# Kernel tuning notes

Hardware: AMD Instinct MI355X
Metric: run time of the kernel (lower is better)

The kernel has to match this reference:

```python
import jax, jax.numpy as jnp
import numpy as np

NB = 5  # number of graph nodes per image
COUNT_THRESH = 10000  # min pixel count for a region to be selected
BOX_DOWNSCALE = 16.0  # backbone stride


def _masks_to_boxes(mask_np, ids):
    # torchvision.ops.masks_to_boxes: (xmin, ymin, xmax, ymax) in pixel coords
    boxes = []
    for oid in ids:
        ys, xs = np.nonzero(mask_np == oid)
        boxes.append([xs.min(), ys.min(), xs.max(), ys.max()])
    return np.asarray(boxes, dtype=np.float32)


def _select_boxes(seg_logits):
    # mask = espnet(x).max(1)[1]; original code only keeps boxes from the LAST
    # batch element (loop variable overwritten each iteration) -- preserved here.
    mask = np.asarray(jnp.argmax(seg_logits, axis=1))[-1]
    ids, counts = np.unique(mask, return_counts=True)
    ids, counts = ids[1:], counts[1:]  # drop background / first label
    boxes = _masks_to_boxes(mask, ids) / BOX_DOWNSCALE  # feature-map coords
    # rr = argsort(argsort(counts, descending)) == rank of each region by size
    rr = np.argsort(np.argsort(-counts))
    sel = []
    for idx in range(len(boxes)):
        for b_idx in range(len(rr)):
            if idx == rr[b_idx] and counts[b_idx] > COUNT_THRESH and len(sel) < NB - 2:
                sel.append(b_idx)
                break
    return boxes.astype(np.int64), sel


def setup_inputs() -> dict:
    key = jax.random.key(0)
    k1, k2, k3 = jax.random.split(key, 3)
    N, K, Hin, Win = 4, 20, 480, 640   # even H/W -> parity padding is a no-op
    C, H, W = 512, Hin // 16, Win // 16  # stride-16 VGG backbone features
    return {
        "seg_logits": jax.random.normal(k1, (N, K, Hin, Win), jnp.float32),
        "feat": jax.random.normal(k2, (N, C, H, W), jnp.float32),
        "pool_x": jax.random.normal(k3, (N, C), jnp.float32),
    }


def reference(seg_logits, feat, pool_x):
    boxes, sel = _select_boxes(seg_logits)
    N, C, H, W = feat.shape
    # Selected-region crops; boxes identical for every batch element (original
    # bug), so each crop+resize is vectorized over the batch dim.
    nodes = []
    for b in sel:
        x0, y0, x1, y1 = [int(v) for v in boxes[b]]
        crop = feat[:, :, y0:y1, x0:x1]
        nodes.append(jax.image.resize(crop, (N, C, H, W), "bilinear"))
    # Fixed fallback boxes (center, left/top/right/bottom strips)
    bb = [[W // 4, H // 4, 3 * W // 4, 3 * H // 4],
          [0, 0, W // 3, H],
          [0, 0, W, H // 3],
          [2 * W // 3, 0, W, H],
          [0, 2 * H // 3, W, H]]
    if len(nodes) < NB:
        for i in range(len(bb) - len(nodes)):  # range evaluated once, as in original
            x0, y0, x1, y1 = bb[i]
            crop = feat[:, :, y0:y1, x0:x1]
            nodes.append(jax.image.resize(crop, (N, C, H, W), "bilinear"))
    graph_nodes = jnp.stack(nodes, axis=1)  # [N, NB, C, H, W]
    # Original: graph_nodes.view(NB, N, ...) is a raw reshape, then cat with feat
    x_cropped = jnp.concatenate(
        [graph_nodes.reshape(NB, N, C, H, W), feat[None]], axis=0)  # [NB+1,N,C,H,W]
    return pool_x, NB, N, x_cropped
```

## Files before the change

kernel.cpp:

```cpp
#include <hip/hip_runtime.h>
#include <hip/hip_bf16.h>

#define K_CLS 20
#define HIN 480
#define WIN 640
#define NPIX (HIN * WIN)
#define C_ 512
#define H_ 30
#define W_ 40
#define NB_ 5
#define CNT_THRESH 10000
#define XCROP_ELEMS (6 * 4 * C_ * H_ * W_)
#define OUT_TOTAL (2050 + XCROP_ELEMS)
#define NPAIR (OUT_TOTAL / 2)

#define NBLK_STATS 300
#define NODE_OFF (NBLK_STATS * 100)


__global__ void stats_k(const float* __restrict__ seg, int* __restrict__ ws) {
    __shared__ int s_cnt[K_CLS], s_mnx[K_CLS], s_mny[K_CLS], s_mxx[K_CLS], s_mxy[K_CLS];
    int t = threadIdx.x;
    if (t < K_CLS) { s_cnt[t] = 0; s_mnx[t] = WIN; s_mny[t] = HIN; s_mxx[t] = -1; s_mxy[t] = -1; }
    __syncthreads();

    int p = blockIdx.x * blockDim.x + t;
    const float4* base = (const float4*)(seg + (size_t)3 * K_CLS * NPIX) + p;
    float4 v = base[0];
    float b0 = v.x, b1 = v.y, b2 = v.z, b3 = v.w;
    int k0 = 0, k1 = 0, k2 = 0, k3 = 0;
    #pragma unroll
    for (int k = 1; k < K_CLS; k++) {
        float4 u = base[(size_t)k * (NPIX / 4)];
        if (u.x > b0) { b0 = u.x; k0 = k; }
        if (u.y > b1) { b1 = u.y; k1 = k; }
        if (u.z > b2) { b2 = u.z; k2 = k; }
        if (u.w > b3) { b3 = u.w; k3 = k; }
    }
    int x = (p * 4) % WIN, y = (p * 4) / WIN;
    if (k0 == k1 && k1 == k2 && k2 == k3) {
        atomicAdd(&s_cnt[k0], 4);
        atomicMin(&s_mnx[k0], x);     atomicMax(&s_mxx[k0], x + 3);
        atomicMin(&s_mny[k0], y);     atomicMax(&s_mxy[k0], y);
    } else {
        int ks[4] = {k0, k1, k2, k3};
        #pragma unroll
        for (int i = 0; i < 4; i++) {
            atomicAdd(&s_cnt[ks[i]], 1);
            atomicMin(&s_mnx[ks[i]], x + i);  atomicMax(&s_mxx[ks[i]], x + i);
            atomicMin(&s_mny[ks[i]], y);      atomicMax(&s_mxy[ks[i]], y);
        }
    }
    __syncthreads();
    if (t < 100) {
        int a = t / 20, c = t % 20;
        int val = (a == 0) ? s_cnt[c] : (a == 1) ? s_mnx[c] : (a == 2) ? s_mny[c]
                : (a == 3) ? s_mxx[c] : s_mxy[c];
        ws[blockIdx.x * 100 + t] = val;
    }
}

__global__ void plan_k(int* __restrict__ ws) {
    __shared__ int part[10][100];
    __shared__ int st[100];
    int t = threadIdx.x;
    if (t < 1000) {
        int c = t % 100, chunk = t / 100;
        int a = c / 20;
        int acc = (a == 0) ? 0 : (a == 1) ? WIN : (a == 2) ? HIN : -1;
        #pragma unroll
        for (int i = 0; i < 30; i++) {
            int v = ws[(chunk * 30 + i) * 100 + c];
            if (a == 0)      acc += v;
            else if (a <= 2) acc = v < acc ? v : acc;
            else             acc = v > acc ? v : acc;
        }
        part[chunk][c] = acc;
    }
    __syncthreads();
    if (t < 100) {
        int a = t / 20;
        int acc = part[0][t];
        #pragma unroll
        for (int i = 1; i < 10; i++) {
            int v = part[i][t];
            if (a == 0)      acc += v;
            else if (a <= 2) acc = v < acc ? v : acc;
            else             acc = v > acc ? v : acc;
        }
        st[t] = acc;
    }
    __syncthreads();
    if (t != 0) return;

    int* cnt = st;
    int* mnx = st + 20; int* mny = st + 40; int* mxx = st + 60; int* mxy = st + 80;
    int* nb  = ws + NODE_OFF;

    int firstp = -1;
    for (int i = 0; i < K_CLS; i++) if (cnt[i] > 0) { firstp = i; break; }
    int order[K_CLS]; int nc = 0;
    for (int i = 0; i < K_CLS; i++)
        if (cnt[i] > 0 && i != firstp) order[nc++] = i;

    for (int i = 1; i < nc; i++) {
        int key = order[i]; int j = i - 1;
        while (j >= 0 && cnt[order[j]] < cnt[key]) { order[j + 1] = order[j]; j--; }
        order[j + 1] = key;
    }

    int nsel = 0;
    for (int i = 0; i < nc && nsel < NB_ - 2; i++) {
        int b = order[i];
        if (cnt[b] > CNT_THRESH) {
            nb[nsel * 4 + 0] = mnx[b] >> 4;
            nb[nsel * 4 + 1] = mny[b] >> 4;
            nb[nsel * 4 + 2] = mxx[b] >> 4;
            nb[nsel * 4 + 3] = mxy[b] >> 4;
            nsel++;
        }
    }
    const int bb[5][4] = {
        {W_ / 4, H_ / 4, 3 * W_ / 4, 3 * H_ / 4},
        {0, 0, W_ / 3, H_},
        {0, 0, W_, H_ / 3},
        {2 * W_ / 3, 0, W_, H_},
        {0, 2 * H_ / 3, W_, H_}
    };
    for (int i = 0; nsel < NB_; i++, nsel++) {
        nb[nsel * 4 + 0] = bb[i][0];
        nb[nsel * 4 + 1] = bb[i][1];
        nb[nsel * 4 + 2] = bb[i][2];
        nb[nsel * 4 + 3] = bb[i][3];
    }
}

__global__ void out_k(const float* __restrict__ feat,
                      const float* __restrict__ pool_x,
                      const int* __restrict__ nb,
                      float* __restrict__ out) {
    int e = blockIdx.x * blockDim.x + threadIdx.x;
    if (e >= NPAIR) return;
    int i0 = e * 2;
    float2* o = (float2*)out + e;
    if (i0 < 2048) { *o = ((const float2*)pool_x)[e]; return; }
    if (i0 == 2048) { *o = make_float2(5.0f, 4.0f); return; }

    int j  = i0 - 2050;
    int w  = j % W_;
    int t1 = j / W_;
    int h  = t1 % H_;
    int t2 = t1 / H_;
    int c  = t2 & (C_ - 1);
    int sn = t2 >> 9;

    if (sn >= 20) {
        int n = sn - 20;
        *o = *(const float2*)(feat + (((size_t)(n * C_ + c) * H_ + h) * W_ + w));
        return;
    }
    int b  = sn % NB_;
    int n2 = sn / NB_;
    int x0 = nb[b * 4 + 0], y0 = nb[b * 4 + 1];
    int x1 = nb[b * 4 + 2], y1 = nb[b * 4 + 3];
    int iw = x1 - x0; if (iw < 1) iw = 1;
    int ih = y1 - y0; if (ih < 1) ih = 1;

    const float* src = feat + (size_t)(n2 * C_ + c) * H_ * W_;

    float fy  = (h + 0.5f) * (float)ih / (float)H_ - 0.5f;
    float flY = floorf(fy);
    float ty  = fy - flY;
    int ylo = (int)flY, yhi = ylo + 1;
    ylo = min(max(ylo, 0), ih - 1);
    yhi = min(max(yhi, 0), ih - 1);
    int r0 = (y0 + ylo) * W_, r1 = (y0 + yhi) * W_;

    float res[2];
    #pragma unroll
    for (int i = 0; i < 2; i++) {
        float fx  = (w + i + 0.5f) * (float)iw / (float)W_ - 0.5f;
        float flX = floorf(fx);
        float tx  = fx - flX;
        int xlo = (int)flX, xhi = xlo + 1;
        xlo = min(max(xlo, 0), iw - 1);
        xhi = min(max(xhi, 0), iw - 1);
        float v00 = src[r0 + x0 + xlo], v01 = src[r0 + x0 + xhi];
        float v10 = src[r1 + x0 + xlo], v11 = src[r1 + x0 + xhi];
        res[i] = (1.0f - ty) * ((1.0f - tx) * v00 + tx * v01)
               +         ty  * ((1.0f - tx) * v10 + tx * v11);
    }
    *o = make_float2(res[0], res[1]);
}

extern "C" void kernel_launch(void* const* d_in, const int* in_sizes, int n_in,
                              void* d_out, int out_size, void* d_ws, size_t ws_size,
                              hipStream_t stream) {
    const float* seg    = (const float*)d_in[0];
    const float* feat   = (const float*)d_in[1];
    const float* pool_x = (const float*)d_in[2];
    float* out = (float*)d_out;
    int* ws = (int*)d_ws;

    stats_k<<<NBLK_STATS, 256, 0, stream>>>(seg, ws);
    plan_k<<<1, 1024, 0, stream>>>(ws);
    out_k<<<(NPAIR + 255) / 256, 256, 0, stream>>>(feat, pool_x, ws + NODE_OFF, out);
}
```

Baseline: 213.9 us.

## Process eight outputs per thread in out_k and move pool_x copy into plan_k

The output kernel now has each thread produce eight consecutive elements, with blocks aligned to a single stacked slice. This reduces per-element index division and block count, and lets the feat copy use float4 loads. The pool_x copy and the two scalar header writes move into the single-block plan kernel. The bilinear math is rewritten in lerp form and the x/y clamps are simplified, which may change rounding slightly. Output stores stay float2 because the 2050-element header leaves the data only 8-byte aligned.

Result: slower. 244.3 us (+14.2%).

```diff
diff --git a/kernel.cpp b/kernel.cpp
--- a/kernel.cpp
+++ b/kernel.cpp
@@ -11,11 +11,17 @@
 #define NB_ 5
 #define CNT_THRESH 10000
 #define XCROP_ELEMS (6 * 4 * C_ * H_ * W_)
+#define ELEMS_PER_SN (C_ * H_ * W_)
 #define OUT_TOTAL (2050 + XCROP_ELEMS)
-#define NPAIR (OUT_TOTAL / 2)
 
 #define NBLK_STATS 300
 #define NODE_OFF (NBLK_STATS * 100)
+
+#define OUT_TPB 256
+#define OUT_EPT 8
+#define OUT_BLK_ELEMS (OUT_TPB * OUT_EPT)
+#define BLKS_PER_SN (ELEMS_PER_SN / OUT_BLK_ELEMS)
+#define OUT_BLOCKS (24 * BLKS_PER_SN)
 
 
 __global__ void stats_k(const float* __restrict__ seg, int* __restrict__ ws) {
@@ -60,10 +66,15 @@
     }
 }
 
-__global__ void plan_k(int* __restrict__ ws) {
+__global__ void plan_k(int* __restrict__ ws, const float* __restrict__ pool_x,
+                       float* __restrict__ out) {
     __shared__ int part[10][100];
     __shared__ int st[100];
     int t = threadIdx.x;
+
+    ((float2*)out)[t] = ((const float2*)pool_x)[t];
+    if (t == 0) { out[2048] = 5.0f; out[2049] = 4.0f; }
+
     if (t < 1000) {
         int c = t % 100, chunk = t / 100;
         int a = c / 20;
@@ -135,62 +146,67 @@
     }
 }
 
-__global__ void out_k(const float* __restrict__ feat,
-                      const float* __restrict__ pool_x,
+__global__ __launch_bounds__(OUT_TPB) void out_k(const float* __restrict__ feat,
                       const int* __restrict__ nb,
                       float* __restrict__ out) {
-    int e = blockIdx.x * blockDim.x + threadIdx.x;
-    if (e >= NPAIR) return;
-    int i0 = e * 2;
-    float2* o = (float2*)out + e;
-    if (i0 < 2048) { *o = ((const float2*)pool_x)[e]; return; }
-    if (i0 == 2048) { *o = make_float2(5.0f, 4.0f); return; }
-
-    int j  = i0 - 2050;
-    int w  = j % W_;
-    int t1 = j / W_;
-    int h  = t1 % H_;
-    int t2 = t1 / H_;
-    int c  = t2 & (C_ - 1);
-    int sn = t2 >> 9;
+    int sn    = blockIdx.x / BLKS_PER_SN;
+    int rbase = (blockIdx.x % BLKS_PER_SN) * OUT_BLK_ELEMS + threadIdx.x * OUT_EPT;
+    float* o  = out + 2050 + (size_t)sn * ELEMS_PER_SN + rbase;
 
     if (sn >= 20) {
-        int n = sn - 20;
-        *o = *(const float2*)(feat + (((size_t)(n * C_ + c) * H_ + h) * W_ + w));
+        const float* src = feat + (size_t)(sn - 20) * ELEMS_PER_SN + rbase;
+        float4 a  = *(const float4*)(src);
+        float4 b4 = *(const float4*)(src + 4);
+        float2* po = (float2*)o;
+        po[0] = make_float2(a.x, a.y);
+        po[1] = make_float2(a.z, a.w);
+        po[2] = make_float2(b4.x, b4.y);
+        po[3] = make_float2(b4.z, b4.w);
         return;
     }
+
     int b  = sn % NB_;
-    int n2 = sn / NB_;
+    int n  = sn / NB_;
     int x0 = nb[b * 4 + 0], y0 = nb[b * 4 + 1];
     int x1 = nb[b * 4 + 2], y1 = nb[b * 4 + 3];
     int iw = x1 - x0; if (iw < 1) iw = 1;
     int ih = y1 - y0; if (ih < 1) ih = 1;
 
-    const float* src = feat + (size_t)(n2 * C_ + c) * H_ * W_;
+    int c  = rbase / (H_ * W_);
+    int r2 = rbase - c * (H_ * W_);
+    int h  = r2 / W_;
+    int w0 = r2 - h * W_;
 
     float fy  = (h + 0.5f) * (float)ih / (float)H_ - 0.5f;
     float flY = floorf(fy);
     float ty  = fy - flY;
-    int ylo = (int)flY, yhi = ylo + 1;
-    ylo = min(max(ylo, 0), ih - 1);
-    yhi = min(max(yhi, 0), ih - 1);
-    int r0 = (y0 + ylo) * W_, r1 = (y0 + yhi) * W_;
-
-    float res[2];
+    int ylo_u = (int)flY;
+    int ylo = max(ylo_u, 0);
+    int yhi = min(ylo_u + 1, ih - 1);
+    int base = (n * C_ + c) * (H_ * W_) + x0;
+    int r0i  = base + (y0 + ylo) * W_;
+    int r1i  = base + (y0 + yhi) * W_;
+
+    float sx = (float)iw * (1.0f / (float)W_);
+    float wc = (float)w0 + 0.5f;
+    float res[OUT_EPT];
     #pragma unroll
-    for (int i = 0; i < 2; i++) {
-        float fx  = (w + i + 0.5f) * (float)iw / (float)W_ - 0.5f;
+    for (int i = 0; i < OUT_EPT; i++) {
+        float fx  = (wc + (float)i) * sx - 0.5f;
         float flX = floorf(fx);
         float tx  = fx - flX;
-        int xlo = (int)flX, xhi = xlo + 1;
-        xlo = min(max(xlo, 0), iw - 1);
-        xhi = min(max(xhi, 0), iw - 1);
-        float v00 = src[r0 + x0 + xlo], v01 = src[r0 + x0 + xhi];
-        float v10 = src[r1 + x0 + xlo], v11 = src[r1 + x0 + xhi];
-        res[i] = (1.0f - ty) * ((1.0f - tx) * v00 + tx * v01)
-               +         ty  * ((1.0f - tx) * v10 + tx * v11);
-    }
-    *o = make_float2(res[0], res[1]);
+        int xlo_u = (int)flX;
+        int xlo = max(xlo_u, 0);
+        int xhi = min(xlo_u + 1, iw - 1);
+        float v00 = feat[r0i + xlo], v01 = feat[r0i + xhi];
+        float v10 = feat[r1i + xlo], v11 = feat[r1i + xhi];
+        float top = v00 + tx * (v01 - v00);
+        float bot = v10 + tx * (v11 - v10);
+        res[i] = top + ty * (bot - top);
+    }
+    float2* po = (float2*)o;
+    #pragma unroll
+    for (int i = 0; i < 4; i++) po[i] = make_float2(res[2 * i], res[2 * i + 1]);
 }
 
 extern "C" void kernel_launch(void* const* d_in, const int* in_sizes, int n_in,
@@ -203,6 +219,6 @@
     int* ws = (int*)d_ws;
 
     stats_k<<<NBLK_STATS, 256, 0, stream>>>(seg, ws);
-    plan_k<<<1, 1024, 0, stream>>>(ws);
-    out_k<<<(NPAIR + 255) / 256, 256, 0, stream>>>(feat, pool_x, ws + NODE_OFF, out);
-}
+    plan_k<<<1, 1024, 0, stream>>>(ws, pool_x, out);
+    out_k<<<OUT_BLOCKS, OUT_TPB, 0, stream>>>(feat, ws + NODE_OFF, out);
+}
```
